# Kernel tuning notes

Hardware: AMD Instinct MI355X
Metric: run time of the kernel (lower is better)

Reference implementation:

```python
import jax, jax.numpy as jnp
import numpy as np

B, C, Z, E = 2, 32, 4, 2
N = C * C * Z  # 4096 grid points per element
P_TH, T_TH = 0.5, 0.5
ELE_D = (0.74, 0.528)


def _consts():
    real_size = jnp.array([25.0, 25.0, 3.0], jnp.float32)
    lattice = real_size / jnp.array([C, C, Z], jnp.float32)
    g = jnp.stack(jnp.meshgrid(jnp.arange(C), jnp.arange(C), jnp.arange(Z), indexing='ij'), axis=-1)
    pit = g.reshape(N, 3).astype(jnp.float32)
    return pit, lattice


def _cdist(a, b):
    # a [M,3], b [K,3] -> [M,K] euclidean distance
    d2 = jnp.sum((a[:, None, :] - b[None, :, :]) ** 2, axis=-1)
    return jnp.sqrt(d2)


def _nms(pos, conf, valid, ele_d):
    # Fixed-shape version of Analyzer.nms: sort by confidence desc (invalid -> -inf, sorts last),
    # triu(<d) adjacency restricted to valid points, matrix-multiply suppression correction.
    key = jnp.where(valid, conf, -jnp.inf)
    order = jnp.argsort(-key)              # descending confidence
    pos_s = pos[order]
    valid_s = valid[order]
    dist = _cdist(pos_s, pos_s)            # [N,N] ~ 64 MB
    iu = jnp.triu(jnp.ones((N, N), bool), k=1)
    adj = ((dist < ele_d) & iu & valid_s[:, None] & valid_s[None, :]).astype(pos.dtype)
    restrain = adj.sum(0)                  # col sums: # earlier neighbors
    restrain_one = (restrain != 0).astype(pos.dtype)
    correct = restrain_one @ adj           # earlier neighbors that are themselves suppressed
    sel = ((restrain - correct) == 0) & valid_s
    keep = jnp.zeros(N, bool).at[order].set(sel)
    return keep & valid


def _match(t_pos, t_valid, p_pos, p_valid, ele_d):
    # TP matching: T point is matched if any valid P within ele_d; argmin gives its P partner.
    dist = _cdist(t_pos, p_pos)            # [N,N]
    dist = jnp.where(t_valid[:, None] & p_valid[None, :], dist, jnp.inf)
    tp_t_mask = (dist < ele_d).any(1)      # rows in torch's TP_T_index
    tp_p_idx = jnp.argmin(dist, axis=1).astype(jnp.int32)  # torch's TP_P_index (valid where tp_t_mask)
    return tp_t_mask, tp_p_idx


def setup_inputs() -> dict:
    key = jax.random.key(0)
    k1, k2 = jax.random.split(key)
    predictions = jax.random.uniform(k1, (B, C, C, Z, E, 4), jnp.float32)
    targets = jax.random.uniform(k2, (B, C, C, Z, E, 4), jnp.float32)
    return {"predictions": predictions, "targets": targets}


def reference(predictions, targets):
    pit, lattice = _consts()
    # [B,C,C,Z,E,4] -> [B,E,N,4]
    pred = predictions.reshape(B, C, C, Z, E, 4).transpose(0, 4, 1, 2, 3, 5).reshape(B, E, N, 4)
    tgt = targets.reshape(B, C, C, Z, E, 4).transpose(0, 4, 1, 2, 3, 5).reshape(B, E, N, 4)

    p_pos = (pred[..., :3] + pit) * lattice    # [B,E,N,3] absolute coords
    p_conf = pred[..., 3]
    mask_p = p_conf > P_TH
    t_pos = (tgt[..., :3] + pit) * lattice
    mask_t = tgt[..., 3] > T_TH

    keeps, tpt, tpp, tptn, tppn = [], [], [], [], []
    for e in range(E):
        d = ELE_D[e]
        keep_e = jax.vmap(lambda p, c, v: _nms(p, c, v, d))(p_pos[:, e], p_conf[:, e], mask_p[:, e])
        tt, tp = jax.vmap(lambda tq, tv, pq, pv: _match(tq, tv, pq, pv, d))(
            t_pos[:, e], mask_t[:, e], p_pos[:, e], mask_p[:, e])
        ttn, tpn = jax.vmap(lambda tq, tv, pq, pv: _match(tq, tv, pq, pv, d))(
            t_pos[:, e], mask_t[:, e], p_pos[:, e], keep_e)
        keeps.append(keep_e); tpt.append(tt); tpp.append(tp); tptn.append(ttn); tppn.append(tpn)

    keep_nms = jnp.stack(keeps, 1)   # [B,E,N] combined mask_p & nms keep
    tp_t_mask = jnp.stack(tpt, 1)
    tp_p_idx = jnp.stack(tpp, 1)
    tp_t_mask_nms = jnp.stack(tptn, 1)
    tp_p_idx_nms = jnp.stack(tppn, 1)

    return (p_pos, mask_p, keep_nms, t_pos, mask_t,
            tp_t_mask, tp_p_idx, tp_t_mask_nms, tp_p_idx_nms)
```

## Files before the change

kernel.cpp:

```cpp
#include <hip/hip_runtime.h>
#include <cmath>
#include <cstdint>

namespace {
constexpr int NPT  = 4096;

constexpr int O_PPOS  = 0;
constexpr int O_MASKP = 49152;
constexpr int O_KEEP  = 65536;
constexpr int O_TPOS  = 81920;
constexpr int O_MASKT = 131072;
constexpr int O_TPT   = 147456;
constexpr int O_TPP   = 163840;
constexpr int O_TPTN  = 180224;
constexpr int O_TPPN  = 196608;

constexpr float GUARD = 1.4999f;
}

__device__ __forceinline__ unsigned long long shfl_xor_u64(unsigned long long v, int m) {
    unsigned lo = (unsigned)v, hi = (unsigned)(v >> 32);
    lo = __shfl_xor(lo, m); hi = __shfl_xor(hi, m);
    return ((unsigned long long)hi << 32) | lo;
}

__device__ __forceinline__ float3 cellpos(float4 p, int n) {
#pragma clang fp contract(off)
    float fx = (float)(n >> 7), fy = (float)((n >> 2) & 31), fz = (float)(n & 3);
    float3 r;
    r.x = (p.x + fx) * 0.78125f;
    r.y = (p.y + fy) * 0.78125f;
    r.z = (p.z + fz) * 0.75f;
    return r;
}
__device__ __forceinline__ float dist2(float3 a, float3 b) {
#pragma clang fp contract(off)
    float dx = a.x - b.x, dy = a.y - b.y, dz = a.z - b.z;
    float d2 = dx * dx + dy * dy;
    return d2 + dz * dz;
}

__device__ __forceinline__ unsigned restrain_of(const float4* __restrict__ pred,
                                                int base4, int pn, float se) {
#pragma clang fp contract(off)
    float4 p = pred[base4 + pn * 2];
    if (!(p.w > 0.5f)) return 0u;
    float3 pj = cellpos(p, pn);
    int gx = pn >> 7, gy = (pn >> 2) & 31;
    unsigned c = 0;
    for (int q = 0; q < 9; ++q) {
        int nx = gx + q / 3 - 1, ny = gy + q % 3 - 1;
        if ((unsigned)nx > 31u || (unsigned)ny > 31u) continue;
        int nb = nx * 128 + ny * 4;
#pragma unroll
        for (int nz = 0; nz < 4; ++nz) {
            int ni = nb + nz;
            float4 pi = pred[base4 + ni * 2];
            float3 qi = cellpos(pi, ni);
            float d2 = dist2(pj, qi);
            bool prec = (pi.w > p.w) || ((pi.w == p.w) && (ni < pn));
            if ((pi.w > 0.5f) && (d2 < se) && prec) c++;
        }
    }
    return c;
}

__device__ __noinline__ bool keep_of(const float4* __restrict__ pred,
                                     int base4, int k, float se) {
#pragma clang fp contract(off)
    float4 p = pred[base4 + k * 2];
    if (!(p.w > 0.5f)) return false;
    float3 pj = cellpos(p, k);
    int gx = k >> 7, gy = (k >> 2) & 31;
    for (int q = 0; q < 9; ++q) {
        int nx = gx + q / 3 - 1, ny = gy + q % 3 - 1;
        if ((unsigned)nx > 31u || (unsigned)ny > 31u) continue;
        int nb = nx * 128 + ny * 4;
        for (int nz = 0; nz < 4; ++nz) {
            int ni = nb + nz;
            float4 pi = pred[base4 + ni * 2];
            float3 qi = cellpos(pi, ni);
            float d2 = dist2(pj, qi);
            bool prec = (pi.w > p.w) || ((pi.w == p.w) && (ni < k));
            if ((pi.w > 0.5f) && (d2 < se) && prec &&
                restrain_of(pred, base4, ni, se) == 0u)
                return false;
        }
    }
    return true;
}

__global__ void __launch_bounds__(512, 4) k_all(const float4* __restrict__ pred,
                                                const float4* __restrict__ tgt,
                                                float* __restrict__ out,
                                                float s0, float s1) {
#pragma clang fp contract(off)
    __shared__ float4 pp[9 * 16 * 4];
    __shared__ unsigned char restr[7 * 14 * 4];
    __shared__ unsigned char keepl[5 * 12 * 4];
    int bid = blockIdx.x;
    int gy0 = (bid & 3) << 3, gx = (bid >> 2) & 31, s = bid >> 7;
    int b = s >> 1, e = s & 1;
    int base4 = b * 8192 + e;
    float se = (s & 1) ? s1 : s0;
    int t = (int)threadIdx.x;

    int rr = t >> 4, hh = t & 15;
    int gyy_c = rr >> 2, z_c = rr & 3;
    int n_c = (gx << 7) + ((gy0 + gyy_c) << 2) + z_c;
    float4 t4 = tgt[base4 + n_c * 2];

    for (int i = t; i < 576; i += 512) {
        int rx = i >> 6, rem = i & 63, ry = rem >> 2, z = rem & 3;
        int px = gx + rx - 4, py = gy0 + ry - 4;
        float4 v = {0.0f, 0.0f, 0.0f, -1.0f};
        if ((unsigned)px < 32u && (unsigned)py < 32u) {
            int pn = px * 128 + py * 4 + z;
            float4 p = pred[base4 + pn * 2];
            float3 c = cellpos(p, pn);
            v.x = c.x; v.y = c.y; v.z = c.z; v.w = p.w;
        }
        pp[i] = v;
    }
    __syncthreads();

    if (t < 392) {
        int ax = t / 56, rem = t - ax * 56, ay = rem >> 2, z = rem & 3;
        int px = gx + ax - 3, py = gy0 + ay - 3;
        float4 p = pp[((ax + 1) * 16 + (ay + 1)) * 4 + z];
        unsigned c = 0;
        if (p.w > 0.5f) {
            int pn = px * 128 + py * 4 + z;
            float3 pj = {p.x, p.y, p.z};
#pragma unroll
            for (int q = 0; q < 9; ++q) {
                int dx = q / 3 - 1, dy = q % 3 - 1;
                int nb = (px + dx) * 128 + (py + dy) * 4;
                const float4* pc = &pp[((ax + 1 + dx) * 16 + (ay + 1 + dy)) * 4];
#pragma unroll
                for (int dz = -1; dz <= 1; ++dz) {
                    int nz = z + dz;
                    int nzc = nz < 0 ? 0 : (nz > 3 ? 3 : nz);
                    float4 pi = pc[nzc];
                    int ni = nb + nz;
                    float3 qi = {pi.x, pi.y, pi.z};
                    float d2 = dist2(pj, qi);
                    bool zok = (unsigned)nz < 4u;
                    bool prec = (pi.w > p.w) || ((pi.w == p.w) && (ni < pn));
                    if (zok && (pi.w > 0.5f) && (d2 < se) && prec) c++;
                }
            }
        }
        restr[t] = (unsigned char)c;
    }
    __syncthreads();

    if (t < 240) {
        int kx = t / 48, rem = t - kx * 48, ky = rem >> 2, z = rem & 3;
        int px = gx + kx - 2, py = gy0 + ky - 2;
        float4 p = pp[((kx + 2) * 16 + (ky + 2)) * 4 + z];
        bool valid = p.w > 0.5f;
        int pn = px * 128 + py * 4 + z;
        unsigned any = 0;
        if (valid) {
            float3 pj = {p.x, p.y, p.z};
#pragma unroll
            for (int q = 0; q < 9; ++q) {
                int dx = q / 3 - 1, dy = q % 3 - 1;
                int nb = (px + dx) * 128 + (py + dy) * 4;
                const float4* pc = &pp[((kx + 2 + dx) * 16 + (ky + 2 + dy)) * 4];
                const unsigned char* lr =
                    &restr[((kx + 1 + dx) * 14 + (ky + 1 + dy)) * 4];
#pragma unroll
                for (int dz = -1; dz <= 1; ++dz) {
                    int nz = z + dz;
                    int nzc = nz < 0 ? 0 : (nz > 3 ? 3 : nz);
                    float4 pi = pc[nzc];
                    int ni = nb + nz;
                    float3 qi = {pi.x, pi.y, pi.z};
                    float d2 = dist2(pj, qi);
                    bool zok = (unsigned)nz < 4u;
                    bool prec = (pi.w > p.w) || ((pi.w == p.w) && (ni < pn));
                    if (zok && (pi.w > 0.5f) && (lr[nzc] == 0) && (d2 < se) && prec)
                        any = 1u;
                }
            }
        }
        bool keep = valid && (any == 0);
        keepl[t] = keep ? 1 : 0;
        if (kx == 2 && ky >= 2 && ky < 10) {
            int row = s * NPT + pn;
            out[O_PPOS + row * 3 + 0] = p.x;
            out[O_PPOS + row * 3 + 1] = p.y;
            out[O_PPOS + row * 3 + 2] = p.z;
            out[O_MASKP + row] = valid ? 1.0f : 0.0f;
            out[O_KEEP + row]  = keep ? 1.0f : 0.0f;
        }
    }
    __syncthreads();

    int gyy = gyy_c, z = z_c, h = hh;
    int gy = gy0 + gyy;
    int n = n_c;
    int row = s * NPT + n;
    float3 tj = cellpos(t4, n);
    bool tv = t4.w > 0.5f;
    if (h == 0) {
        out[O_TPOS + row * 3 + 0] = tj.x;
        out[O_TPOS + row * 3 + 1] = tj.y;
        out[O_TPOS + row * 3 + 2] = tj.z;
        out[O_MASKT + row] = tv ? 1.0f : 0.0f;
    }
    if (!tv) {
        if (h == 0) {
            out[O_TPT + row] = 0.0f; out[O_TPTN + row] = 0.0f;
            out[O_TPP + row] = 0.0f; out[O_TPPN + row] = 0.0f;
        }
        return;
    }
    unsigned long long bs = ~0ull, bn = ~0ull;
    unsigned as_ = 0, an_ = 0;
#pragma unroll
    for (int pass = 0; pass < 2; ++pass) {
        int q = pass * 16 + h;
        if (q > 24) continue;
        int dx = q / 5 - 2, dy = q % 5 - 2;
        int nb = (gx + dx) * 128 + (gy + dy) * 4;
        const float4* pc = &pp[((dx + 4) * 16 + (gyy + dy + 4)) * 4];
        const unsigned char* lk = &keepl[((dx + 2) * 12 + (gyy + dy + 2)) * 4];
#pragma unroll
        for (int nz = 0; nz < 4; ++nz) {
            float4 pi = pc[nz];
            int ni = nb + nz;
            float3 qi = {pi.x, pi.y, pi.z};
            float d2 = dist2(tj, qi);
            float dist = sqrtf(d2);
            unsigned long long enc =
                ((unsigned long long)__float_as_uint(dist) << 32) | (unsigned)ni;
            if (pi.w > 0.5f) { if (enc < bs) bs = enc; if (d2 < se) as_ = 1u; }
            if (lk[nz]) { if (enc < bn) bn = enc; if (d2 < se) an_ = 1u; }
        }
    }
    for (int m = 1; m < 16; m <<= 1) {
        unsigned long long o = shfl_xor_u64(bs, m); if (o < bs) bs = o;
        o = shfl_xor_u64(bn, m); if (o < bn) bn = o;
        as_ |= __shfl_xor(as_, m);
        an_ |= __shfl_xor(an_, m);
    }
    bool acc_s = __uint_as_float((unsigned)(bs >> 32)) < GUARD;
    bool acc_n = __uint_as_float((unsigned)(bn >> 32)) < GUARD;
    if (!(acc_s && acc_n)) {
        unsigned long long fs = ~0ull, fn = ~0ull;
        for (int k = h; k < NPT; k += 16) {
            float4 pi = pred[base4 + k * 2];
            float3 qi = cellpos(pi, k);
            float d2 = dist2(tj, qi);
            float dist = sqrtf(d2);
            unsigned long long enc =
                ((unsigned long long)__float_as_uint(dist) << 32) | (unsigned)k;
            if (pi.w > 0.5f && enc < fs) fs = enc;
            if (enc < fn && keep_of(pred, base4, k, se)) fn = enc;
        }
        for (int m = 1; m < 16; m <<= 1) {
            unsigned long long o = shfl_xor_u64(fs, m); if (o < fs) fs = o;
            o = shfl_xor_u64(fn, m); if (o < fn) fn = o;
        }
        bs = fs; bn = fn;
    }
    if (h == 0) {
        out[O_TPT + row]  = as_ ? 1.0f : 0.0f;
        out[O_TPTN + row] = an_ ? 1.0f : 0.0f;
        out[O_TPP + row]  = (float)((bs == ~0ull) ? 0u : (unsigned)(bs & 0xffffffffull));
        out[O_TPPN + row] = (float)((bn == ~0ull) ? 0u : (unsigned)(bn & 0xffffffffull));
    }
}

static float sq_boundary(float t) {
    float f = (float)((double)t * (double)t);
    while (sqrtf(f) >= t) f = nextafterf(f, 0.0f);
    while (sqrtf(f) < t)  f = nextafterf(f, __builtin_inff());
    return f;
}

extern "C" void kernel_launch(void* const* d_in, const int* in_sizes, int n_in,
                              void* d_out, int out_size, void* d_ws, size_t ws_size,
                              hipStream_t stream) {
    (void)in_sizes; (void)n_in; (void)out_size; (void)d_ws; (void)ws_size;
    const float4* pred = (const float4*)d_in[0];
    const float4* tgt  = (const float4*)d_in[1];
    float* out = (float*)d_out;

    float s0 = sq_boundary(0.74f);
    float s1 = sq_boundary(0.528f);

    k_all<<<dim3(512), dim3(512), 0, stream>>>(pred, tgt, out, s0, s1);
}
```

Baseline: 64.85 us.

## Halve per-block tile height, double grid, and use 32 lanes per target point

Each block now covers 4 y-cells instead of 8, so the grid grows from 512 to 1024 blocks, with smaller shared halo arrays and launch bounds raised to 8 blocks per CU. Matching now gives each target point 32 lanes, so all 25 neighbour cells are handled in one pass and the fallback full scan uses a stride of 32. The target-output and pred-output writes move earlier or onto idle threads. This adds parallelism and occupancy, at the cost of a larger halo overhead relative to the interior (more redundant cellpos and restrain work per useful point).

```diff
diff --git a/kernel.cpp b/kernel.cpp
--- a/kernel.cpp
+++ b/kernel.cpp
@@ -90,28 +90,37 @@
     return true;
 }
 
-__global__ void __launch_bounds__(512, 4) k_all(const float4* __restrict__ pred,
+__global__ void __launch_bounds__(512, 8) k_all(const float4* __restrict__ pred,
                                                 const float4* __restrict__ tgt,
                                                 float* __restrict__ out,
                                                 float s0, float s1) {
 #pragma clang fp contract(off)
-    __shared__ float4 pp[9 * 16 * 4];
-    __shared__ unsigned char restr[7 * 14 * 4];
-    __shared__ unsigned char keepl[5 * 12 * 4];
+    __shared__ float4 pp[9 * 12 * 4];
+    __shared__ unsigned char restr[7 * 10 * 4];
+    __shared__ unsigned char keepl[5 * 8 * 4];
     int bid = blockIdx.x;
-    int gy0 = (bid & 3) << 3, gx = (bid >> 2) & 31, s = bid >> 7;
+    int gy0 = (bid & 7) << 2, gx = (bid >> 3) & 31, s = bid >> 8;
     int b = s >> 1, e = s & 1;
     int base4 = b * 8192 + e;
     float se = (s & 1) ? s1 : s0;
     int t = (int)threadIdx.x;
 
-    int rr = t >> 4, hh = t & 15;
+    int rr = t >> 5, hh = t & 31;
     int gyy_c = rr >> 2, z_c = rr & 3;
     int n_c = (gx << 7) + ((gy0 + gyy_c) << 2) + z_c;
+    int row_c = s * NPT + n_c;
     float4 t4 = tgt[base4 + n_c * 2];
-
-    for (int i = t; i < 576; i += 512) {
-        int rx = i >> 6, rem = i & 63, ry = rem >> 2, z = rem & 3;
+    float3 tj = cellpos(t4, n_c);
+    bool tv = t4.w > 0.5f;
+    if (hh == 0) {
+        out[O_TPOS + row_c * 3 + 0] = tj.x;
+        out[O_TPOS + row_c * 3 + 1] = tj.y;
+        out[O_TPOS + row_c * 3 + 2] = tj.z;
+        out[O_MASKT + row_c] = tv ? 1.0f : 0.0f;
+    }
+
+    if (t < 432) {
+        int rx = t / 48, rem = t - rx * 48, ry = rem >> 2, z = rem & 3;
         int px = gx + rx - 4, py = gy0 + ry - 4;
         float4 v = {0.0f, 0.0f, 0.0f, -1.0f};
         if ((unsigned)px < 32u && (unsigned)py < 32u) {
@@ -120,14 +129,14 @@
             float3 c = cellpos(p, pn);
             v.x = c.x; v.y = c.y; v.z = c.z; v.w = p.w;
         }
-        pp[i] = v;
+        pp[t] = v;
     }
     __syncthreads();
 
-    if (t < 392) {
-        int ax = t / 56, rem = t - ax * 56, ay = rem >> 2, z = rem & 3;
+    if (t < 280) {
+        int ax = t / 40, rem = t - ax * 40, ay = rem >> 2, z = rem & 3;
         int px = gx + ax - 3, py = gy0 + ay - 3;
-        float4 p = pp[((ax + 1) * 16 + (ay + 1)) * 4 + z];
+        float4 p = pp[((ax + 1) * 12 + (ay + 1)) * 4 + z];
         unsigned c = 0;
         if (p.w > 0.5f) {
             int pn = px * 128 + py * 4 + z;
@@ -136,7 +145,7 @@
             for (int q = 0; q < 9; ++q) {
                 int dx = q / 3 - 1, dy = q % 3 - 1;
                 int nb = (px + dx) * 128 + (py + dy) * 4;
-                const float4* pc = &pp[((ax + 1 + dx) * 16 + (ay + 1 + dy)) * 4];
+                const float4* pc = &pp[((ax + 1 + dx) * 12 + (ay + 1 + dy)) * 4];
 #pragma unroll
                 for (int dz = -1; dz <= 1; ++dz) {
                     int nz = z + dz;
@@ -152,13 +161,23 @@
             }
         }
         restr[t] = (unsigned char)c;
+    } else if (t >= 448 && t < 464) {
+        int ir = t - 448;
+        int gyy = ir >> 2, z = ir & 3;
+        int n = (gx << 7) + ((gy0 + gyy) << 2) + z;
+        int row = s * NPT + n;
+        float4 p = pp[(48 + (gyy + 4)) * 4 + z];
+        out[O_PPOS + row * 3 + 0] = p.x;
+        out[O_PPOS + row * 3 + 1] = p.y;
+        out[O_PPOS + row * 3 + 2] = p.z;
+        out[O_MASKP + row] = (p.w > 0.5f) ? 1.0f : 0.0f;
     }
     __syncthreads();
 
-    if (t < 240) {
-        int kx = t / 48, rem = t - kx * 48, ky = rem >> 2, z = rem & 3;
+    if (t < 160) {
+        int kx = t / 32, rem = t - kx * 32, ky = rem >> 2, z = rem & 3;
         int px = gx + kx - 2, py = gy0 + ky - 2;
-        float4 p = pp[((kx + 2) * 16 + (ky + 2)) * 4 + z];
+        float4 p = pp[((kx + 2) * 12 + (ky + 2)) * 4 + z];
         bool valid = p.w > 0.5f;
         int pn = px * 128 + py * 4 + z;
         unsigned any = 0;
@@ -168,9 +187,9 @@
             for (int q = 0; q < 9; ++q) {
                 int dx = q / 3 - 1, dy = q % 3 - 1;
                 int nb = (px + dx) * 128 + (py + dy) * 4;
-                const float4* pc = &pp[((kx + 2 + dx) * 16 + (ky + 2 + dy)) * 4];
+                const float4* pc = &pp[((kx + 2 + dx) * 12 + (ky + 2 + dy)) * 4];
                 const unsigned char* lr =
-                    &restr[((kx + 1 + dx) * 14 + (ky + 1 + dy)) * 4];
+                    &restr[((kx + 1 + dx) * 10 + (ky + 1 + dy)) * 4];
 #pragma unroll
                 for (int dz = -1; dz <= 1; ++dz) {
                     int nz = z + dz;
@@ -188,29 +207,16 @@
         }
         bool keep = valid && (any == 0);
         keepl[t] = keep ? 1 : 0;
-        if (kx == 2 && ky >= 2 && ky < 10) {
+        if (kx == 2 && ky >= 2 && ky < 6) {
             int row = s * NPT + pn;
-            out[O_PPOS + row * 3 + 0] = p.x;
-            out[O_PPOS + row * 3 + 1] = p.y;
-            out[O_PPOS + row * 3 + 2] = p.z;
-            out[O_MASKP + row] = valid ? 1.0f : 0.0f;
-            out[O_KEEP + row]  = keep ? 1.0f : 0.0f;
+            out[O_KEEP + row] = keep ? 1.0f : 0.0f;
         }
     }
     __syncthreads();
 
-    int gyy = gyy_c, z = z_c, h = hh;
+    int gyy = gyy_c, h = hh;
     int gy = gy0 + gyy;
-    int n = n_c;
-    int row = s * NPT + n;
-    float3 tj = cellpos(t4, n);
-    bool tv = t4.w > 0.5f;
-    if (h == 0) {
-        out[O_TPOS + row * 3 + 0] = tj.x;
-        out[O_TPOS + row * 3 + 1] = tj.y;
-        out[O_TPOS + row * 3 + 2] = tj.z;
-        out[O_MASKT + row] = tv ? 1.0f : 0.0f;
-    }
+    int row = row_c;
     if (!tv) {
         if (h == 0) {
             out[O_TPT + row] = 0.0f; out[O_TPTN + row] = 0.0f;
@@ -220,14 +226,11 @@
     }
     unsigned long long bs = ~0ull, bn = ~0ull;
     unsigned as_ = 0, an_ = 0;
-#pragma unroll
-    for (int pass = 0; pass < 2; ++pass) {
-        int q = pass * 16 + h;
-        if (q > 24) continue;
-        int dx = q / 5 - 2, dy = q % 5 - 2;
+    if (h < 25) {
+        int dx = h / 5 - 2, dy = h % 5 - 2;
         int nb = (gx + dx) * 128 + (gy + dy) * 4;
-        const float4* pc = &pp[((dx + 4) * 16 + (gyy + dy + 4)) * 4];
-        const unsigned char* lk = &keepl[((dx + 2) * 12 + (gyy + dy + 2)) * 4];
+        const float4* pc = &pp[((dx + 4) * 12 + (gyy + dy + 4)) * 4];
+        const unsigned char* lk = &keepl[((dx + 2) * 8 + (gyy + dy + 2)) * 4];
 #pragma unroll
         for (int nz = 0; nz < 4; ++nz) {
             float4 pi = pc[nz];
@@ -241,7 +244,7 @@
             if (lk[nz]) { if (enc < bn) bn = enc; if (d2 < se) an_ = 1u; }
         }
     }
-    for (int m = 1; m < 16; m <<= 1) {
+    for (int m = 1; m < 32; m <<= 1) {
         unsigned long long o = shfl_xor_u64(bs, m); if (o < bs) bs = o;
         o = shfl_xor_u64(bn, m); if (o < bn) bn = o;
         as_ |= __shfl_xor(as_, m);
@@ -251,7 +254,7 @@
     bool acc_n = __uint_as_float((unsigned)(bn >> 32)) < GUARD;
     if (!(acc_s && acc_n)) {
         unsigned long long fs = ~0ull, fn = ~0ull;
-        for (int k = h; k < NPT; k += 16) {
+        for (int k = h; k < NPT; k += 32) {
             float4 pi = pred[base4 + k * 2];
             float3 qi = cellpos(pi, k);
             float d2 = dist2(tj, qi);
@@ -261,7 +264,7 @@
             if (pi.w > 0.5f && enc < fs) fs = enc;
             if (enc < fn && keep_of(pred, base4, k, se)) fn = enc;
         }
-        for (int m = 1; m < 16; m <<= 1) {
+        for (int m = 1; m < 32; m <<= 1) {
             unsigned long long o = shfl_xor_u64(fs, m); if (o < fs) fs = o;
             o = shfl_xor_u64(fn, m); if (o < fn) fn = o;
         }
@@ -293,5 +296,5 @@
     float s0 = sq_boundary(0.74f);
     float s1 = sq_boundary(0.528f);
 
-    k_all<<<dim3(512), dim3(512), 0, stream>>>(pred, tgt, out, s0, s1);
-}
+    k_all<<<dim3(1024), dim3(512), 0, stream>>>(pred, tgt, out, s0, s1);
+}
```

Result: slower. 118.2 us (+82.3%).
